# Optimization experiments

Measured on AMD Instinct MI355X. Metric: run time of the kernel, lower is better.

## Reference

```python
import jax, jax.numpy as jnp
import numpy as np


def complex_relu(v):
    # mask by sign of real part, applied to the full complex value
    return (v.real >= 0) * v


def magnetic_laplacian(senders, receivers, n_node, n_nodes, q=0.25):
    """Symmetric-normalized magnetic Laplacian, [b, n, n] complex64.

    Faithful to the source with default q_absolute=0.25 (truthy), so the
    `else` branch (constant q per graph) is taken.
    """
    b = senders.shape[0]
    edges_padding_mask = (senders >= 0).astype(jnp.float32)  # [b, e]
    # adj[b, s, r] += mask[s]  (faithful scatter, incl. the d[s] gather)
    def assign(a, s, r, d):
        return a.at[s, r].add(d[s])
    adj = jax.vmap(assign)(
        jnp.zeros((b, n_nodes, n_nodes), jnp.float32),
        senders, receivers, edges_padding_mask)
    adj = jnp.where(adj > 1, 1.0, adj)
    adj_t = jnp.swapaxes(adj, -1, -2)
    sym_adj = adj + adj_t
    sym_adj = jnp.where((adj != 0) & (adj_t != 0), sym_adj / 2, sym_adj)
    sym_deg = sym_adj.sum(-2)  # [b, n]
    qv = jnp.full(b, q, dtype=jnp.float32)  # q_absolute branch
    theta = 1j * 2 * jnp.pi * qv[:, None, None] * (adj - adj_t)
    # diagonal D^{-1/2}; diag-matmul expressed as row/col scaling (same math)
    inv_sqrt_deg = jax.lax.rsqrt(jnp.clip(sym_deg, 1))  # [b, n]
    norm_adj = inv_sqrt_deg[:, :, None] * sym_adj * inv_sqrt_deg[:, None, :]
    laplacian = jnp.eye(n_nodes) - norm_adj * jnp.exp(theta)
    idx = jnp.arange(n_nodes)[None, :]  # [1, n]
    node_mask = idx < n_node[:, :1]  # [b, n]
    pair_mask = node_mask[:, :, None] * node_mask[:, None, :]  # [b, n, n]
    return pair_mask * laplacian


def _magnet_forward(nodes, senders, receivers, n_node,
                    w0_0, b0_0, w1_0, w0_1, b0_1, w1_1):
    b, n, d = nodes.shape
    lap = magnetic_laplacian(senders, receivers, n_node, n)
    max_eigenvalue = jnp.linalg.eigvalsh(lap).max()  # scalar over batch
    eye = jnp.eye(n, dtype=lap.dtype)
    t_1 = (2.0 / max_eigenvalue) * lap - eye[None]  # [b, n, n] complex
    x = nodes + 0j  # complex64 state
    for w0, b0, w1 in ((w0_0, b0_0, w1_0), (w0_1, b0_1, w1_1)):
        # t_0 = I, so t_0 @ x == x
        x_0 = (x.real @ w0 + b0) + 1j * (x.imag @ w0 + b0)
        x_t1 = t_1 @ x  # [b, n, d] complex
        x_1 = (x_t1.real @ w1) + 1j * (x_t1.imag @ w1)
        x = complex_relu(x_0 + x_1)
    return jnp.concatenate((x.real, x.imag), axis=-1)  # [b, n, 2*d_model]


def setup_inputs() -> dict:
    key = jax.random.key(0)
    ks = jax.random.split(key, 10)
    b, n, e, d = 64, 512, 4096, 256
    scale = 1.0 / np.sqrt(d)
    return {
        "nodes": jax.random.normal(ks[0], (b, n, d), jnp.float32),
        "senders": jax.random.randint(ks[1], (b, e), 0, n, dtype=jnp.int32),
        "receivers": jax.random.randint(ks[2], (b, e), 0, n, dtype=jnp.int32),
        "n_node": jax.random.randint(ks[3], (b, 1), 0, n, dtype=jnp.int32),
        "w0_0": jax.random.normal(ks[4], (d, d), jnp.float32) * scale,
        "b0_0": jnp.zeros((d,), jnp.float32),
        "w1_0": jax.random.normal(ks[5], (d, d), jnp.float32) * scale,
        "w0_1": jax.random.normal(ks[6], (d, d), jnp.float32) * scale,
        "b0_1": jnp.zeros((d,), jnp.float32),
        "w1_1": jax.random.normal(ks[7], (d, d), jnp.float32) * scale,
    }


def reference(nodes, senders, receivers, n_node,
              w0_0, b0_0, w1_0, w0_1, b0_1, w1_1):
    return _magnet_forward(nodes, senders, receivers, n_node,
                           w0_0, b0_0, w1_0, w0_1, b0_1, w1_1)
```

## Files before the change

### kernel.cpp

```cpp
#include <hip/hip_runtime.h>
#include <stdint.h>

typedef unsigned long long u64;
typedef unsigned int u32;
typedef unsigned short u16;

#define BATCH 64
#define NN    512
#define NAUG  1024
#define DM    256
#define NEDGE 4096
#define CAP   64
#define PK2   32
#define PK2A  36
#define LM    128

#define OFF_ADJ   ((size_t)0)
#define SZ_ADJ    ((size_t)BATCH*NN*8*8)
#define OFF_ADJT  (OFF_ADJ + SZ_ADJ)
#define OFF_LAM   (OFF_ADJT + SZ_ADJ)
#define OFF_LMX   (OFF_LAM + 64)
#define OFF_PK2   (OFF_LAM + 1024)
#define SZ_PK2    ((size_t)BATCH*PK2A*NN*16)
#define OFF_DEGI  (OFF_PK2 + SZ_PK2)
#define OFF_LENS  (OFF_DEGI + (size_t)BATCH*NN*4)
#define OFF_ENTS  (OFF_LENS + (size_t)BATCH*NN*4)
#define OFF_VALS  (OFF_ENTS + (size_t)BATCH*NN*CAP*4)
#define OFF_XF    (OFF_VALS + (size_t)BATCH*NN*CAP*4)
#define OFF_XT1   (OFF_XF  + (size_t)BATCH*NAUG*DM*4)
#define OFF_S     (OFF_XT1 + (size_t)BATCH*NAUG*DM*4)

__global__ void k_scatter(const int* __restrict__ senders, const int* __restrict__ receivers,
                          u64* __restrict__ adj, u64* __restrict__ adjT){
    int idx = blockIdx.x * 256 + threadIdx.x;
    int b = idx >> 12;
    int s = senders[idx];
    int r = receivers[idx];
    if (s >= 0){
        atomicOr(&adj [((size_t)b*NN + s)*8 + (r >> 6)], 1ull << (r & 63));
        atomicOr(&adjT[((size_t)b*NN + r)*8 + (s >> 6)], 1ull << (s & 63));
    }
}

__global__ void k_deg(const u64* __restrict__ adj, const u64* __restrict__ adjT,
                      float* __restrict__ degInv){
    int idx = blockIdx.x * 256 + threadIdx.x;
    const u64* a = adj  + (size_t)idx * 8;
    const u64* t = adjT + (size_t)idx * 8;
    int deg = 0;
#pragma unroll
    for (int w = 0; w < 8; ++w) deg += __popcll(a[w] | t[w]);
    degInv[idx] = (float)(1.0 / sqrt((double)(deg < 1 ? 1 : deg)));
}

__global__ __launch_bounds__(256)
void k_build(const u64* __restrict__ adj, const u64* __restrict__ adjT,
             const float* __restrict__ degInv, const int* __restrict__ n_node,
             u32* __restrict__ ents, float* __restrict__ vals, int* __restrict__ lens,
             uint2* __restrict__ pk2, int* __restrict__ lmax){
    int gw   = (blockIdx.x * 256 + threadIdx.x) >> 6;
    int lane = threadIdx.x & 63;
    int b = gw >> 9;
    int i = gw & (NN - 1);
    const u64* arow = adj  + ((size_t)b*NN + i)*8;
    const u64* trow = adjT + ((size_t)b*NN + i)*8;
    int wsel = lane >> 3, sh = (lane & 7) * 8;
    u32 ba = (u32)((arow[wsel] >> sh) & 0xFFull);
    u32 bt = (u32)((trow[wsel] >> sh) & 0xFFull);
    int nn_b = n_node[b];
    bool mi  = i < nn_b;
    float di = degInv[b*NN + i];
    int j0 = lane * 8;

    float vr_[8], vi_[8];
    int cnt = 0;
#pragma unroll
    for (int jj = 0; jj < 8; ++jj){
        int j = j0 + jj;
        int a = (ba >> jj) & 1, t = (bt >> jj) & 1;
        bool mm = mi && (j < nn_b);
        float c = di * degInv[b*NN + j];
        float vr = 0.f, vi = 0.f;
        if (j == i){
            if (mm) vr = 1.0f - (a ? c : 0.0f);
        } else if (mm && ((a | t) != 0)){
            if (a & t)      vr = -c;
            else if (a)     vi = -c;
            else            vi =  c;
        }
        vr_[jj] = vr; vi_[jj] = vi;
        cnt += (vr != 0.f || vi != 0.f) ? 1 : 0;
    }
    int off = cnt;
#pragma unroll
    for (int d = 1; d < 64; d <<= 1){
        int nb = __shfl_up(off, d);
        if (lane >= d) off += nb;
    }
    int excl = off - cnt;
    int tot  = __shfl(off, 63);
    int p = excl;
    u32*   erow = ents + ((size_t)b*NN + i)*CAP;
    float* vrow = vals + ((size_t)b*NN + i)*CAP;
#pragma unroll
    for (int jj = 0; jj < 8; ++jj){
        float vr = vr_[jj], vi = vi_[jj];
        if (vr != 0.f || vi != 0.f){
            if (p < CAP){
                int ty = (vi != 0.f) ? 1 : 0;
                int j = j0 + jj;
                float v = ty ? vi : vr;
                erow[p] = (u32)j | ((u32)ty << 9);
                vrow[p] = v;
                size_t slot = ((size_t)b*PK2A + (p >> 1))*NN + i;
                pk2[slot*2 + (p & 1)] =
                    make_uint2((u32)((j << 3) + (ty << 12)), __float_as_uint(v));
            }
            p++;
        }
    }
    if (lane == 63){
        int tc = tot > CAP ? CAP : tot;
        lens[b*NN + i] = tc;
        atomicMax(&lmax[b], tc);
    }
}

#define DO_G4(S0)                                                         \
    {                                                                     \
        float2 vva = VALS[S0][tid];                                       \
        float2 vvb = VALS[S0+1][tid];                                     \
        u32 opa = offp[S0], opb = offp[S0+1];                             \
        float2 u0 = *(const float2*)((const char*)XY + (opa & 0xFFFFu));  \
        float2 u1 = *(const float2*)((const char*)XY + (opa >> 16));      \
        float2 u2 = *(const float2*)((const char*)XY + (opb & 0xFFFFu));  \
        float2 u3 = *(const float2*)((const char*)XY + (opb >> 16));      \
        wr0 = fmaf(vva.x, u0.x, wr0); wi0 = fmaf(vva.x, u0.y, wi0);       \
        wr0 = fmaf(vva.y, u1.x, wr0); wi0 = fmaf(vva.y, u1.y, wi0);       \
        wr1 = fmaf(vvb.x, u2.x, wr1); wi1 = fmaf(vvb.x, u2.y, wi1);       \
        wr1 = fmaf(vvb.y, u3.x, wr1); wi1 = fmaf(vvb.y, u3.y, wi1);       \
        float2 vvc = VALS[S0+2][tid];                                     \
        float2 vvd = VALS[S0+3][tid];                                     \
        u32 opc = offp[S0+2], opd = offp[S0+3];                           \
        float2 u4 = *(const float2*)((const char*)XY + (opc & 0xFFFFu));  \
        float2 u5 = *(const float2*)((const char*)XY + (opc >> 16));      \
        float2 u6 = *(const float2*)((const char*)XY + (opd & 0xFFFFu));  \
        float2 u7 = *(const float2*)((const char*)XY + (opd >> 16));      \
        wr0 = fmaf(vvc.x, u4.x, wr0); wi0 = fmaf(vvc.x, u4.y, wi0);       \
        wr0 = fmaf(vvc.y, u5.x, wr0); wi0 = fmaf(vvc.y, u5.y, wi0);       \
        wr1 = fmaf(vvd.x, u6.x, wr1); wi1 = fmaf(vvd.x, u6.y, wi1);       \
        wr1 = fmaf(vvd.y, u7.x, wr1); wi1 = fmaf(vvd.y, u7.y, wi1);       \
    }

__global__ __launch_bounds__(512)
void k_lanczos(const uint4* __restrict__ pk2, const int* __restrict__ lens,
               float* __restrict__ lam){
    int b = blockIdx.x;
    int tid = threadIdx.x;
    int w = tid >> 6, l = tid & 63;
    __shared__ float2 XY[2*NN];
    __shared__ float2 VALS[PK2][NN];
    __shared__ float alphS[LM], betS[LM];
    __shared__ float redA[8], redB[8];
    __shared__ int bCnt[PK2 + 1], bOff[PK2 + 1];
    __shared__ u16 sortRow[NN];
    const uint4* base = pk2 + (size_t)b*PK2A*NN;

    if (tid <= PK2) bCnt[tid] = 0;
    __syncthreads();
    int defES = (lens[b*NN + tid] + 1) >> 1;
    atomicAdd(&bCnt[defES], 1);
    __syncthreads();
    if (tid == 0){
        int acc = 0;
        for (int e = PK2; e >= 0; --e){ bOff[e] = acc; acc += bCnt[e]; }
    }
    __syncthreads();
    int pos = atomicAdd(&bOff[defES], 1);
    sortRow[pos] = (u16)tid;
    __syncthreads();
    int row  = sortRow[tid];
    int myES = (lens[b*NN + row] + 1) >> 1;

    u32 offp[PK2];
#pragma unroll
    for (int s = 0; s < PK2; ++s){
        uint4 q = base[(size_t)s*NN + row];
        offp[s] = (q.x & 0xFFFFu) | (q.z << 16);
        VALS[s][tid] = make_float2(__uint_as_float(q.y), __uint_as_float(q.w));
    }

    u32 h = (u32)row * 2654435761u + 0x9E3779B9u;
    h ^= h >> 16; h *= 0x85EBCA6Bu; h ^= h >> 13;
    float xr = (float)(h & 0xFFFF) * (1.f/65536.f) - 0.5f;
    h = h * 1664525u + 1013904223u;
    float xi = (float)(h & 0xFFFF) * (1.f/65536.f) - 0.5f;
    float ss = xr*xr + xi*xi;
#pragma unroll
    for (int d = 1; d < 64; d <<= 1) ss += __shfl_xor(ss, d);
    if (l == 0) redA[w] = ss;
    __syncthreads();
    float inv0 = 1.f / sqrtf(redA[0] + redA[1] + redA[2] + redA[3]
                           + redA[4] + redA[5] + redA[6] + redA[7]);
    xr *= inv0; xi *= inv0;
    XY[row]      = make_float2(xr, xi);
    XY[NN + row] = make_float2(-xi, xr);
    __syncthreads();
    float v0r = 0.f, v0i = 0.f;
    float betaPrev = 0.f;
    int mEff = LM;
    for (int j = 0; j < LM; ++j){
        float wr0 = 0.f, wi0 = 0.f, wr1 = 0.f, wi1 = 0.f;
        if (myES >  0) DO_G4(0);
        if (myES >  4) DO_G4(4);
        if (myES >  8) DO_G4(8);
        if (myES > 12) DO_G4(12);
        if (myES > 16) DO_G4(16);
        if (myES > 20) DO_G4(20);
        if (myES > 24) DO_G4(24);
        if (myES > 28) DO_G4(28);
        float wr = wr0 + wr1, wi = wi0 + wi1;
        float pa = xr*wr + xi*wi;
#pragma unroll
        for (int d = 1; d < 64; d <<= 1) pa += __shfl_xor(pa, d);
        if (l == 0) redA[w] = pa;
        __syncthreads();
        float paF = redA[0] + redA[1] + redA[2] + redA[3]
                  + redA[4] + redA[5] + redA[6] + redA[7];
        wr -= paF*xr + betaPrev*v0r;
        wi -= paF*xi + betaPrev*v0i;
        float pb = wr*wr + wi*wi;
#pragma unroll
        for (int d = 1; d < 64; d <<= 1) pb += __shfl_xor(pb, d);
        if (l == 0) redB[w] = pb;
        __syncthreads();
        float pbF = redB[0] + redB[1] + redB[2] + redB[3]
                  + redB[4] + redB[5] + redB[6] + redB[7];
        float bta = sqrtf(pbF);
        if (w == 0 && l == 0){ alphS[j] = paF; betS[j] = bta; }
        if (pbF < 1e-14f){ mEff = j + 1; break; }
        float binv = 1.f / bta;
        float nr = wr * binv;
        float ni = wi * binv;
        v0r = xr; v0i = xi;
        xr = nr; xi = ni;
        XY[row]      = make_float2(nr, ni);
        XY[NN + row] = make_float2(-ni, nr);
        __syncthreads();
        betaPrev = bta;
    }
    if (w == 0){
        int m = mEff;
        double lo = -0.5, hi = 2.5;
        for (int sweep = 0; sweep < 5; ++sweep){
            double wd = (hi - lo) * (1.0/65.0);
            double mid = lo + wd * (double)(l + 1);
            int cnt = 0;
            double d = (double)alphS[0] - mid;
            if (d < 0.0) cnt++;
            for (int k = 1; k < m; ++k){
                if (d == 0.0) d = -1e-300;
                double bk = (double)betS[k-1];
                d = ((double)alphS[k] - mid) - bk*bk/d;
                if (d < 0.0) cnt++;
            }
            u64 mask = __ballot(cnt >= m);
            if (mask == 0ull){
                lo = lo + wd * 64.0;
            } else {
                int L = __ffsll(mask) - 1;
                hi = lo + wd * (double)(L + 1);
                lo = lo + wd * (double)L;
            }
        }
        if (l == 0){
            float l1 = (float)hi;
            if (l1 < 0.f) l1 = 0.f;
            if (l1 > 2.0f) l1 = 2.0f;
            atomicMax((u32*)lam, __float_as_uint(l1));
        }
    }
}

__global__ void k_prep32(const float* __restrict__ nodes, float* __restrict__ xf){
    int row = blockIdx.x;
    int t = threadIdx.x;
    int b = row >> 10, i = row & (NAUG - 1);
    float v = (i < NN) ? nodes[((size_t)b*NN + i)*DM + t] : 0.f;
    xf[(size_t)row*DM + t] = v;
}

__global__ __launch_bounds__(256)
void k_spmm(const u32* __restrict__ ents, const float* __restrict__ vals,
            const int* __restrict__ lens, const float* __restrict__ xf,
            const float* __restrict__ lam, float* __restrict__ xt1){
    int i = blockIdx.x;
    int b = blockIdx.y;
    int t = threadIdx.x;
    int len = lens[b*NN + i];
    const u32*   er = ents + ((size_t)b*NN + i)*CAP;
    const float* ev = vals + ((size_t)b*NN + i)*CAP;
    const float* xb = xf + (size_t)b*NAUG*DM;
    double ar = 0.0, ai = 0.0;
    for (int e = 0; e < len; ++e){
        u32 en = er[e];
        double v = (double)ev[e];
        int j = en & 511;
        double xr = (double)xb[(size_t)j*DM + t];
        double xi = (double)xb[(size_t)(NN + j)*DM + t];
        if (en & 512u){ ar = fma(v, -xi, ar); ai = fma(v, xr, ai); }
        else          { ar = fma(v,  xr, ar); ai = fma(v, xi, ai); }
    }
    double alpha = 2.0 / (double)lam[0];
    size_t ro = ((size_t)b*NAUG + i)*DM + t;
    size_t io = ((size_t)b*NAUG + NN + i)*DM + t;
    xt1[ro] = (float)(alpha*ar - (double)xf[ro]);
    xt1[io] = (float)(alpha*ai - (double)xf[io]);
}

__global__ __launch_bounds__(256)
void k_gemm32(const float* __restrict__ A0, const float* __restrict__ xt1,
              const float* __restrict__ w0, const float* __restrict__ w1,
              const float* __restrict__ bias, float* __restrict__ dst,
              int rowStride, int imagOff){
    __shared__ float As[32][68];
    __shared__ float Bs[32][68];
    int h  = blockIdx.x;
    int bx = (h >> 3) & 3;
    int by = ((h >> 5) << 3) | (h & 7);
    int b  = by >> 4;
    int i0 = (by & 15) * 32;
    int n0 = bx * 64;
    int tid = threadIdx.x;
    int tx = tid & 15, ty = tid >> 4;
    size_t abase = (size_t)b*NAUG*DM;
    double acc[4][4];
#pragma unroll
    for (int r = 0; r < 4; ++r)
#pragma unroll
        for (int c = 0; c < 4; ++c) acc[r][c] = 0.0;
    for (int ph = 0; ph < 2; ++ph){
        const float* A = ph ? xt1 : A0;
        const float* W = ph ? w1 : w0;
        for (int k0 = 0; k0 < DM; k0 += 32){
#pragma unroll
            for (int l = 0; l < 2; ++l){
                int fi = tid + l*256;
                int m  = fi >> 3, c4 = fi & 7;
                size_t grow = abase + (size_t)((m & 1)*NN + i0 + (m >> 1))*DM;
                float4 g = *(const float4*)(A + grow + k0 + c4*4);
                int pc = ((((m >> 2) ^ c4) << 2) | (m & 3));
                As[c4*4+0][pc] = g.x; As[c4*4+1][pc] = g.y;
                As[c4*4+2][pc] = g.z; As[c4*4+3][pc] = g.w;
                int kk = fi >> 4, n4 = fi & 15;
                float4 hh = *(const float4*)(W + ((size_t)(k0 + kk))*DM + n0 + n4*4);
                *(float4*)&Bs[kk][n4*4] = hh;
            }
            __syncthreads();
            float facc[4][4];
#pragma unroll
            for (int r = 0; r < 4; ++r)
#pragma unroll
                for (int c = 0; c < 4; ++c) facc[r][c] = 0.f;
#pragma unroll
            for (int kk = 0; kk < 32; ++kk){
                float4 a4 = *(const float4*)&As[kk][((ty ^ ((kk >> 2) & 7)) << 2)];
                float4 b4 = *(const float4*)&Bs[kk][tx*4];
                facc[0][0] = fmaf(a4.x, b4.x, facc[0][0]);
                facc[0][1] = fmaf(a4.x, b4.y, facc[0][1]);
                facc[0][2] = fmaf(a4.x, b4.z, facc[0][2]);
                facc[0][3] = fmaf(a4.x, b4.w, facc[0][3]);
                facc[1][0] = fmaf(a4.y, b4.x, facc[1][0]);
                facc[1][1] = fmaf(a4.y, b4.y, facc[1][1]);
                facc[1][2] = fmaf(a4.y, b4.z, facc[1][2]);
                facc[1][3] = fmaf(a4.y, b4.w, facc[1][3]);
                facc[2][0] = fmaf(a4.z, b4.x, facc[2][0]);
                facc[2][1] = fmaf(a4.z, b4.y, facc[2][1]);
                facc[2][2] = fmaf(a4.z, b4.z, facc[2][2]);
                facc[2][3] = fmaf(a4.z, b4.w, facc[2][3]);
                facc[3][0] = fmaf(a4.w, b4.x, facc[3][0]);
                facc[3][1] = fmaf(a4.w, b4.y, facc[3][1]);
                facc[3][2] = fmaf(a4.w, b4.z, facc[3][2]);
                facc[3][3] = fmaf(a4.w, b4.w, facc[3][3]);
            }
#pragma unroll
            for (int r = 0; r < 4; ++r)
#pragma unroll
                for (int c = 0; c < 4; ++c) acc[r][c] += (double)facc[r][c];
            __syncthreads();
        }
    }
    float4 bi = *(const float4*)(bias + n0 + tx*4);
    float* outb = dst + (size_t)b*NAUG*DM;
#pragma unroll
    for (int q = 0; q < 2; ++q){
        float4 re, im;
        re.x = (float)(acc[q*2][0]   + (double)bi.x);
        re.y = (float)(acc[q*2][1]   + (double)bi.y);
        re.z = (float)(acc[q*2][2]   + (double)bi.z);
        re.w = (float)(acc[q*2][3]   + (double)bi.w);
        im.x = (float)(acc[q*2+1][0] + (double)bi.x);
        im.y = (float)(acc[q*2+1][1] + (double)bi.y);
        im.z = (float)(acc[q*2+1][2] + (double)bi.z);
        im.w = (float)(acc[q*2+1][3] + (double)bi.w);
        float4 gr, gi;
        gr.x = (re.x >= 0.f) ? re.x : 0.f;  gi.x = (re.x >= 0.f) ? im.x : 0.f;
        gr.y = (re.y >= 0.f) ? re.y : 0.f;  gi.y = (re.y >= 0.f) ? im.y : 0.f;
        gr.z = (re.z >= 0.f) ? re.z : 0.f;  gi.z = (re.z >= 0.f) ? im.z : 0.f;
        gr.w = (re.w >= 0.f) ? re.w : 0.f;  gi.w = (re.w >= 0.f) ? im.w : 0.f;
        int i = i0 + ty*2 + q;
        float* pre = outb + (size_t)i*rowStride + n0 + tx*4;
        *(float4*)pre            = gr;
        *(float4*)(pre + imagOff) = gi;
    }
}

extern "C" void kernel_launch(void* const* d_in, const int* in_sizes, int n_in,
                              void* d_out, int out_size, void* d_ws, size_t ws_size,
                              hipStream_t stream){
    const float* nodes   = (const float*)d_in[0];
    const int*   senders = (const int*)  d_in[1];
    const int*   recvs   = (const int*)  d_in[2];
    const int*   n_node  = (const int*)  d_in[3];
    const float* w00     = (const float*)d_in[4];
    const float* b00     = (const float*)d_in[5];
    const float* w10     = (const float*)d_in[6];
    const float* w01     = (const float*)d_in[7];
    const float* b01     = (const float*)d_in[8];
    const float* w11     = (const float*)d_in[9];
    char* ws = (char*)d_ws;
    u64*   adj    = (u64*)  (ws + OFF_ADJ);
    u64*   adjT   = (u64*)  (ws + OFF_ADJT);
    float* lam    = (float*)(ws + OFF_LAM);
    int*   lmax   = (int*)  (ws + OFF_LMX);
    uint2* pk2    = (uint2*)(ws + OFF_PK2);
    float* degInv = (float*)(ws + OFF_DEGI);
    int*   lens   = (int*)  (ws + OFF_LENS);
    u32*   ents   = (u32*)  (ws + OFF_ENTS);
    float* vals   = (float*)(ws + OFF_VALS);
    float* xf     = (float*)(ws + OFF_XF);
    float* xt1    = (float*)(ws + OFF_XT1);
    float* xf2    = (float*)(ws + OFF_S);
    float* out    = (float*)d_out;

    hipMemsetAsync(ws + OFF_ADJ, 0, OFF_PK2 + SZ_PK2, stream);

    k_scatter<<<dim3(BATCH*NEDGE/256), dim3(256), 0, stream>>>(senders, recvs, adj, adjT);
    k_deg    <<<dim3(BATCH*NN/256),    dim3(256), 0, stream>>>(adj, adjT, degInv);
    k_build  <<<dim3(BATCH*NN/4),      dim3(256), 0, stream>>>(adj, adjT, degInv, n_node,
                                                               ents, vals, lens, pk2, lmax);
    k_lanczos<<<dim3(BATCH),           dim3(512), 0, stream>>>((const uint4*)pk2, lens, lam);
    k_prep32 <<<dim3(BATCH*NAUG),      dim3(256), 0, stream>>>(nodes, xf);

    k_spmm  <<<dim3(NN, BATCH),        dim3(256), 0, stream>>>(ents, vals, lens, xf, lam, xt1);
    k_gemm32<<<dim3(4096),             dim3(256), 0, stream>>>(xf, xt1, w00, w10, b00,
                                                               xf2, DM, NN*DM);
    k_spmm  <<<dim3(NN, BATCH),        dim3(256), 0, stream>>>(ents, vals, lens, xf2, lam, xt1);
    k_gemm32<<<dim3(4096),             dim3(256), 0, stream>>>(xf2, xt1, w01, w11, b01,
                                                               out, 2*DM, DM);
}
```

Before: 1.140 ms.

## Split Lanczos SpMV across two thread halves with 1024-thread blocks

The Lanczos kernel now launches 1024 threads per batch block. Each row's packed nonzero slots are split between two threads, one taking the even slots and one the odd slots. The second half writes its partial product to shared memory, and the first half combines it and does the reductions and the vector update. The goal is to shorten the latency-bound serial Lanczos iterations by halving the gather work per thread and raising occupancy, at the cost of an extra barrier per iteration and idle threads during the reduction phases.

```diff
diff --git a/kernel.cpp b/kernel.cpp
--- a/kernel.cpp
+++ b/kernel.cpp
@@ -126,40 +126,30 @@
     }
 }
 
-#define DO_G4(S0)                                                         \
+#define DO_GH(K0)                                                         \
     {                                                                     \
-        float2 vva = VALS[S0][tid];                                       \
-        float2 vvb = VALS[S0+1][tid];                                     \
-        u32 opa = offp[S0], opb = offp[S0+1];                             \
-        float2 u0 = *(const float2*)((const char*)XY + (opa & 0xFFFFu));  \
-        float2 u1 = *(const float2*)((const char*)XY + (opa >> 16));      \
-        float2 u2 = *(const float2*)((const char*)XY + (opb & 0xFFFFu));  \
-        float2 u3 = *(const float2*)((const char*)XY + (opb >> 16));      \
-        wr0 = fmaf(vva.x, u0.x, wr0); wi0 = fmaf(vva.x, u0.y, wi0);       \
-        wr0 = fmaf(vva.y, u1.x, wr0); wi0 = fmaf(vva.y, u1.y, wi0);       \
-        wr1 = fmaf(vvb.x, u2.x, wr1); wi1 = fmaf(vvb.x, u2.y, wi1);       \
-        wr1 = fmaf(vvb.y, u3.x, wr1); wi1 = fmaf(vvb.y, u3.y, wi1);       \
-        float2 vvc = VALS[S0+2][tid];                                     \
-        float2 vvd = VALS[S0+3][tid];                                     \
-        u32 opc = offp[S0+2], opd = offp[S0+3];                           \
-        float2 u4 = *(const float2*)((const char*)XY + (opc & 0xFFFFu));  \
-        float2 u5 = *(const float2*)((const char*)XY + (opc >> 16));      \
-        float2 u6 = *(const float2*)((const char*)XY + (opd & 0xFFFFu));  \
-        float2 u7 = *(const float2*)((const char*)XY + (opd >> 16));      \
-        wr0 = fmaf(vvc.x, u4.x, wr0); wi0 = fmaf(vvc.x, u4.y, wi0);       \
-        wr0 = fmaf(vvc.y, u5.x, wr0); wi0 = fmaf(vvc.y, u5.y, wi0);       \
-        wr1 = fmaf(vvd.x, u6.x, wr1); wi1 = fmaf(vvd.x, u6.y, wi1);       \
-        wr1 = fmaf(vvd.y, u7.x, wr1); wi1 = fmaf(vvd.y, u7.y, wi1);       \
-    }
-
-__global__ __launch_bounds__(512)
+        _Pragma("unroll")                                                 \
+        for (int k = K0; k < K0 + 4; ++k){                                \
+            float2 vv = VALS[half + 2*k][st];                             \
+            u32 op = offp[k];                                             \
+            float2 u0 = *(const float2*)((const char*)XY + (op & 0xFFFFu)); \
+            float2 u1 = *(const float2*)((const char*)XY + (op >> 16));   \
+            wr = fmaf(vv.x, u0.x, wr); wi = fmaf(vv.x, u0.y, wi);         \
+            wr = fmaf(vv.y, u1.x, wr); wi = fmaf(vv.y, u1.y, wi);         \
+        }                                                                 \
+    }
+
+__global__ __launch_bounds__(1024)
 void k_lanczos(const uint4* __restrict__ pk2, const int* __restrict__ lens,
                float* __restrict__ lam){
     int b = blockIdx.x;
     int tid = threadIdx.x;
+    int half = tid >> 9;
+    int st   = tid & 511;
     int w = tid >> 6, l = tid & 63;
     __shared__ float2 XY[2*NN];
     __shared__ float2 VALS[PK2][NN];
+    __shared__ float2 WH[NN];
     __shared__ float alphS[LM], betS[LM];
     __shared__ float redA[8], redB[8];
     __shared__ int bCnt[PK2 + 1], bOff[PK2 + 1];
@@ -168,84 +158,103 @@
 
     if (tid <= PK2) bCnt[tid] = 0;
     __syncthreads();
-    int defES = (lens[b*NN + tid] + 1) >> 1;
-    atomicAdd(&bCnt[defES], 1);
+    if (half == 0){
+        int defES = (lens[b*NN + st] + 1) >> 1;
+        atomicAdd(&bCnt[defES], 1);
+    }
     __syncthreads();
     if (tid == 0){
         int acc = 0;
         for (int e = PK2; e >= 0; --e){ bOff[e] = acc; acc += bCnt[e]; }
     }
     __syncthreads();
-    int pos = atomicAdd(&bOff[defES], 1);
-    sortRow[pos] = (u16)tid;
-    __syncthreads();
-    int row  = sortRow[tid];
+    if (half == 0){
+        int defES = (lens[b*NN + st] + 1) >> 1;
+        int pos = atomicAdd(&bOff[defES], 1);
+        sortRow[pos] = (u16)st;
+    }
+    __syncthreads();
+    int row  = sortRow[st];
     int myES = (lens[b*NN + row] + 1) >> 1;
-
-    u32 offp[PK2];
-#pragma unroll
-    for (int s = 0; s < PK2; ++s){
-        uint4 q = base[(size_t)s*NN + row];
-        offp[s] = (q.x & 0xFFFFu) | (q.z << 16);
-        VALS[s][tid] = make_float2(__uint_as_float(q.y), __uint_as_float(q.w));
-    }
-
-    u32 h = (u32)row * 2654435761u + 0x9E3779B9u;
-    h ^= h >> 16; h *= 0x85EBCA6Bu; h ^= h >> 13;
-    float xr = (float)(h & 0xFFFF) * (1.f/65536.f) - 0.5f;
-    h = h * 1664525u + 1013904223u;
-    float xi = (float)(h & 0xFFFF) * (1.f/65536.f) - 0.5f;
-    float ss = xr*xr + xi*xi;
-#pragma unroll
-    for (int d = 1; d < 64; d <<= 1) ss += __shfl_xor(ss, d);
-    if (l == 0) redA[w] = ss;
-    __syncthreads();
-    float inv0 = 1.f / sqrtf(redA[0] + redA[1] + redA[2] + redA[3]
-                           + redA[4] + redA[5] + redA[6] + redA[7]);
-    xr *= inv0; xi *= inv0;
-    XY[row]      = make_float2(xr, xi);
-    XY[NN + row] = make_float2(-xi, xr);
+    int myK  = (myES - half + 1) >> 1;
+    if (myES == 0) myK = 0;
+
+    u32 offp[16];
+#pragma unroll
+    for (int k = 0; k < 16; ++k){
+        uint4 q = base[(size_t)(half + 2*k)*NN + row];
+        offp[k] = (q.x & 0xFFFFu) | (q.z << 16);
+        VALS[half + 2*k][st] = make_float2(__uint_as_float(q.y), __uint_as_float(q.w));
+    }
+
+    float xr = 0.f, xi = 0.f;
+    if (half == 0){
+        u32 h = (u32)row * 2654435761u + 0x9E3779B9u;
+        h ^= h >> 16; h *= 0x85EBCA6Bu; h ^= h >> 13;
+        xr = (float)(h & 0xFFFF) * (1.f/65536.f) - 0.5f;
+        h = h * 1664525u + 1013904223u;
+        xi = (float)(h & 0xFFFF) * (1.f/65536.f) - 0.5f;
+        float ss = xr*xr + xi*xi;
+#pragma unroll
+        for (int d = 1; d < 64; d <<= 1) ss += __shfl_xor(ss, d);
+        if (l == 0) redA[w] = ss;
+    }
+    __syncthreads();
+    if (half == 0){
+        float inv0 = 1.f / sqrtf(redA[0] + redA[1] + redA[2] + redA[3]
+                               + redA[4] + redA[5] + redA[6] + redA[7]);
+        xr *= inv0; xi *= inv0;
+        XY[row]      = make_float2(xr, xi);
+        XY[NN + row] = make_float2(-xi, xr);
+    }
     __syncthreads();
     float v0r = 0.f, v0i = 0.f;
     float betaPrev = 0.f;
     int mEff = LM;
     for (int j = 0; j < LM; ++j){
-        float wr0 = 0.f, wi0 = 0.f, wr1 = 0.f, wi1 = 0.f;
-        if (myES >  0) DO_G4(0);
-        if (myES >  4) DO_G4(4);
-        if (myES >  8) DO_G4(8);
-        if (myES > 12) DO_G4(12);
-        if (myES > 16) DO_G4(16);
-        if (myES > 20) DO_G4(20);
-        if (myES > 24) DO_G4(24);
-        if (myES > 28) DO_G4(28);
-        float wr = wr0 + wr1, wi = wi0 + wi1;
-        float pa = xr*wr + xi*wi;
-#pragma unroll
-        for (int d = 1; d < 64; d <<= 1) pa += __shfl_xor(pa, d);
-        if (l == 0) redA[w] = pa;
+        float wr = 0.f, wi = 0.f;
+        if (myK >  0) DO_GH(0);
+        if (myK >  4) DO_GH(4);
+        if (myK >  8) DO_GH(8);
+        if (myK > 12) DO_GH(12);
+        if (half == 1) WH[st] = make_float2(wr, wi);
         __syncthreads();
-        float paF = redA[0] + redA[1] + redA[2] + redA[3]
-                  + redA[4] + redA[5] + redA[6] + redA[7];
-        wr -= paF*xr + betaPrev*v0r;
-        wi -= paF*xi + betaPrev*v0i;
-        float pb = wr*wr + wi*wi;
-#pragma unroll
-        for (int d = 1; d < 64; d <<= 1) pb += __shfl_xor(pb, d);
-        if (l == 0) redB[w] = pb;
+        float paF = 0.f;
+        if (half == 0){
+            float2 wo = WH[st];
+            wr = wr + wo.x;
+            wi = wi + wo.y;
+            float pa = xr*wr + xi*wi;
+#pragma unroll
+            for (int d = 1; d < 64; d <<= 1) pa += __shfl_xor(pa, d);
+            if (l == 0) redA[w] = pa;
+        }
+        __syncthreads();
+        if (half == 0){
+            paF = redA[0] + redA[1] + redA[2] + redA[3]
+                + redA[4] + redA[5] + redA[6] + redA[7];
+            wr -= paF*xr + betaPrev*v0r;
+            wi -= paF*xi + betaPrev*v0i;
+            float pb = wr*wr + wi*wi;
+#pragma unroll
+            for (int d = 1; d < 64; d <<= 1) pb += __shfl_xor(pb, d);
+            if (l == 0) redB[w] = pb;
+        }
         __syncthreads();
         float pbF = redB[0] + redB[1] + redB[2] + redB[3]
                   + redB[4] + redB[5] + redB[6] + redB[7];
         float bta = sqrtf(pbF);
-        if (w == 0 && l == 0){ alphS[j] = paF; betS[j] = bta; }
+        if (tid == 0){ alphS[j] = paF; betS[j] = bta; }
         if (pbF < 1e-14f){ mEff = j + 1; break; }
-        float binv = 1.f / bta;
-        float nr = wr * binv;
-        float ni = wi * binv;
-        v0r = xr; v0i = xi;
-        xr = nr; xi = ni;
-        XY[row]      = make_float2(nr, ni);
-        XY[NN + row] = make_float2(-ni, nr);
+        if (half == 0){
+            float binv = 1.f / bta;
+            float nr = wr * binv;
+            float ni = wi * binv;
+            v0r = xr; v0i = xi;
+            xr = nr; xi = ni;
+            XY[row]      = make_float2(nr, ni);
+            XY[NN + row] = make_float2(-ni, nr);
+        }
         __syncthreads();
         betaPrev = bta;
     }
@@ -449,7 +458,7 @@
     k_deg    <<<dim3(BATCH*NN/256),    dim3(256), 0, stream>>>(adj, adjT, degInv);
     k_build  <<<dim3(BATCH*NN/4),      dim3(256), 0, stream>>>(adj, adjT, degInv, n_node,
                                                                ents, vals, lens, pk2, lmax);
-    k_lanczos<<<dim3(BATCH),           dim3(512), 0, stream>>>((const uint4*)pk2, lens, lam);
+    k_lanczos<<<dim3(BATCH),           dim3(1024), 0, stream>>>((const uint4*)pk2, lens, lam);
     k_prep32 <<<dim3(BATCH*NAUG),      dim3(256), 0, stream>>>(nodes, xf);
 
     k_spmm  <<<dim3(NN, BATCH),        dim3(256), 0, stream>>>(ents, vals, lens, xf, lam, xt1);
```

Result: no change. 1.142 ms (+0.1%).
